# Kernel optimization log

Measured on AMD Instinct MI355X. Metric: run time of the kernel, lower is better.

## Reference

```python
import jax, jax.numpy as jnp
import numpy as np

P = 8  # patch_size hard-coded in the module


def conv1x1(x, W, b):
    # x: [B,C,H,W_], W: [O,C], b: [O]  (1x1 conv == per-pixel linear)
    return jnp.einsum('oc,bchw->bohw', W, x) + b[None, :, None, None]


def to_patch_tokens(t):
    # Replicates t.unfold(2,P,P).unfold(3,P,P).contiguous().view(B,-1,N)
    # t: [B,Cq,W,H] -> [B, Cq*P*P, N] with N = (W//P)*(H//P)
    B, Cq, Wd, Hd = t.shape
    Wp, Hp = Wd // P, Hd // P
    t = t.reshape(B, Cq, Wp, P, Hp, P).transpose(0, 1, 2, 4, 3, 5)  # [B,Cq,Wp,Hp,P,P]
    return t.reshape(B, Cq * P * P, Wp * Hp)


def setup_inputs() -> dict:
    key = jax.random.key(0)
    ks = jax.random.split(key, 10)
    B, C, Wd, Hd = 8, 64, 256, 256
    Cq = C // 8
    s_in = 1.0 / np.sqrt(C)
    s_out = 1.0 / np.sqrt(Cq)
    return {
        'x': jax.random.normal(ks[0], (B, C, Wd, Hd), jnp.float32),
        'Wq': jax.random.normal(ks[1], (Cq, C), jnp.float32) * s_in,
        'bq': jax.random.normal(ks[2], (Cq,), jnp.float32) * 0.01,
        'Wk': jax.random.normal(ks[3], (Cq, C), jnp.float32) * s_in,
        'bk': jax.random.normal(ks[4], (Cq,), jnp.float32) * 0.01,
        'Wv': jax.random.normal(ks[5], (Cq, C), jnp.float32) * s_in,
        'bv': jax.random.normal(ks[6], (Cq,), jnp.float32) * 0.01,
        'Wo': jax.random.normal(ks[7], (C, Cq), jnp.float32) * s_out,
        'bo': jax.random.normal(ks[8], (C,), jnp.float32) * 0.01,
        'gamma': jax.random.normal(ks[9], (1,), jnp.float32),
    }


def reference(x, Wq, bq, Wk, bk, Wv, bv, Wo, bo, gamma):
    B, C, Wd, Hd = x.shape
    Cq = C // 8
    q = to_patch_tokens(conv1x1(x, Wq, bq)).transpose(0, 2, 1)  # [B,N,M]
    k = to_patch_tokens(conv1x1(x, Wk, bk))                     # [B,M,N]
    v = to_patch_tokens(conv1x1(x, Wv, bv))                     # [B,M,N]
    N = k.shape[-1]  # d_k in source == number of patch tokens
    energy = jnp.einsum('bnm,bmk->bnk', q, k) / jnp.sqrt(jnp.float32(N))
    attn = jax.nn.softmax(energy, axis=-1)                      # [B,N,N]
    out = jnp.einsum('bmn,bjn->bmj', v, attn)                   # bmm(v, attn^T)
    out = out.transpose(0, 2, 1).reshape(B, Cq, Wd, Hd)
    out = conv1x1(out, Wo, bo)
    return gamma * out + x
```

## Files before the change

### kernel.cpp

```cpp
#include <hip/hip_runtime.h>
#include <stdint.h>

typedef unsigned short u16;
typedef unsigned int   u32;
typedef __attribute__((ext_vector_type(8))) short  short8;
typedef __attribute__((ext_vector_type(4))) float  floatx4;

__device__ __forceinline__ u16 f32_to_bf16(float f) {
  u32 u = __builtin_bit_cast(u32, f);
  u = (u + 0x7fffu + ((u >> 16) & 1u)) >> 16;
  return (u16)u;
}
__device__ __forceinline__ float bf16_to_f32(u16 h) {
  u32 u = ((u32)h) << 16;
  return __builtin_bit_cast(float, u);
}
__device__ __forceinline__ float bf16_lo(u32 u) {
  return __builtin_bit_cast(float, u << 16);
}
__device__ __forceinline__ float bf16_hi(u32 u) {
  return __builtin_bit_cast(float, u & 0xffff0000u);
}

__device__ __forceinline__ void load_lds16(const u16* g, u16* l) {
  auto gp = (const __attribute__((address_space(1))) u32*)(uintptr_t)g;
  auto lp = (__attribute__((address_space(3))) u32*)(u32)(uintptr_t)l;
  __builtin_amdgcn_global_load_lds(gp, lp, 16, 0, 0);
}

__global__ __launch_bounds__(512) void qkv_kernel(
    const float* __restrict__ x,
    const float* __restrict__ Wq, const float* __restrict__ bq,
    const float* __restrict__ Wk, const float* __restrict__ bk,
    const float* __restrict__ Wv, const float* __restrict__ bv,
    u16* __restrict__ qt, u16* __restrict__ kt, u16* __restrict__ vm)
{
  __shared__ __align__(16) u16 qs[128 * 64];
  __shared__ __align__(16) u16 ks_[128 * 64];
  __shared__ __align__(16) u16 vs[64 * 128];

  const int wq = blockIdx.x;
  const int g  = blockIdx.y;
  const int b  = blockIdx.z;
  const int t  = threadIdx.x;
  const int vt0 = t << 1;
  const int lw = vt0 >> 5, lh = vt0 & 31;
  const int w  = wq * 32 + lw;
  const int h  = g * 16 + (lh & 15) + ((lh >> 4) << 7);
  const int nl = ((lh >> 3) & 1) * 64 + (lw & 7) * 8 + (lh & 7);
  const int mc = ((lw >> 3) << 1) + (lh >> 4);

  float aq[2][8], ak[2][8], av[2][8];
#pragma unroll
  for (int j = 0; j < 2; j++)
#pragma unroll
    for (int i = 0; i < 8; i++) { aq[j][i] = 0.f; ak[j][i] = 0.f; av[j][i] = 0.f; }

  const float* xp = x + (size_t)b * 64 * 65536 + w * 256 + h;
#pragma unroll 4
  for (int c = 0; c < 64; c++) {
    float2 xv = *(const float2*)(xp + c * 65536);
#pragma unroll
    for (int cq = 0; cq < 8; cq++) {
      float wqc = Wq[cq * 64 + c], wkc = Wk[cq * 64 + c], wvc = Wv[cq * 64 + c];
      aq[0][cq] = fmaf(wqc, xv.x, aq[0][cq]);
      ak[0][cq] = fmaf(wkc, xv.x, ak[0][cq]);
      av[0][cq] = fmaf(wvc, xv.x, av[0][cq]);
      aq[1][cq] = fmaf(wqc, xv.y, aq[1][cq]);
      ak[1][cq] = fmaf(wkc, xv.y, ak[1][cq]);
      av[1][cq] = fmaf(wvc, xv.y, av[1][cq]);
    }
  }
#pragma unroll
  for (int j = 0; j < 2; j++)
#pragma unroll
    for (int cq = 0; cq < 8; cq++) {
      qs[(nl + j) * 64 + cq * 8 + mc]    = f32_to_bf16(aq[j][cq] + bq[cq]);
      ks_[(nl + j) * 64 + cq * 8 + mc]   = f32_to_bf16(ak[j][cq] + bk[cq]);
      vs[(cq * 8 + mc) * 128 + nl + j]   = f32_to_bf16(av[j][cq] + bv[cq]);
    }
  __syncthreads();

#pragma unroll
  for (int i = 0; i < 2; i++) {
    const int vt = t + i * 512;
    {
      const int nl2 = vt >> 3, cq2 = vt & 7;
      const size_t row = (size_t)b * 1024 + g * 128 + nl2;
      uint4 vq = *(const uint4*)(qs + nl2 * 64 + cq2 * 8);
      uint4 vk = *(const uint4*)(ks_ + nl2 * 64 + cq2 * 8);
      *(uint4*)(qt + row * 512 + cq2 * 64 + wq * 8) = vq;
      *(uint4*)(kt + row * 512 + cq2 * 64 + wq * 8) = vk;
    }
    {
      const int pr = vt >> 4, l16 = vt & 15;
      const int cq3 = pr >> 3, mc3 = pr & 7;
      const int mrow = cq3 * 64 + wq * 8 + mc3;
      uint4 vv = *(const uint4*)(vs + pr * 128 + l16 * 8);
      *(uint4*)(vm + ((size_t)b * 512 + mrow) * 1024 + g * 128 + l16 * 8) = vv;
    }
  }
}

template <int FMW>
__global__ __launch_bounds__(256) void gemm_nt(
    const u16* __restrict__ A, const u16* __restrict__ Bm, u16* __restrict__ Cm,
    int M, int N, int K, float scale)
{
  constexpr int BM = FMW * 32;
  __shared__ __align__(16) u16 As[BM * 64];
  __shared__ __align__(16) u16 Bs[128 * 64];

  const int bn = blockIdx.x, bm = blockIdx.y, bz = blockIdx.z;
  const int t = threadIdx.x;
  const int lane = t & 63, wid = t >> 6;
  const int wm = wid & 1, wn = wid >> 1;
  const int m0 = bm * BM, n0 = bn * 128;

  const u16* Ab = A + (size_t)bz * M * K + (size_t)m0 * K;
  const u16* Bb = Bm + (size_t)bz * N * K + (size_t)n0 * K;

  floatx4 acc[FMW][4];
#pragma unroll
  for (int i = 0; i < FMW; i++)
#pragma unroll
    for (int j = 0; j < 4; j++) acc[i][j] = (floatx4){0.f, 0.f, 0.f, 0.f};

  const int srow = wid * 8 + (lane >> 3);
  const int scol = (((lane & 7) ^ ((lane >> 3) & 7)) << 3);
  const int l15 = lane & 15, quad = lane >> 4;
  const int cxor = (l15 & 7) << 3;

  for (int k0 = 0; k0 < K; k0 += 64) {
#pragma unroll
    for (int i = 0; i < FMW; i++)
      load_lds16(Ab + (size_t)(i * 32 + srow) * K + k0 + scol, As + (i * 32 + wid * 8) * 64);
#pragma unroll
    for (int i = 0; i < 4; i++)
      load_lds16(Bb + (size_t)(i * 32 + srow) * K + k0 + scol, Bs + (i * 32 + wid * 8) * 64);
    __syncthreads();
#pragma unroll
    for (int ks = 0; ks < 2; ks++) {
      const int koff = (ks * 32 + quad * 8) ^ cxor;
      short8 a[FMW], b[4];
#pragma unroll
      for (int f = 0; f < FMW; f++)
        a[f] = *(const short8*)(As + (wm * FMW * 16 + f * 16 + l15) * 64 + koff);
#pragma unroll
      for (int f = 0; f < 4; f++)
        b[f] = *(const short8*)(Bs + (wn * 64 + f * 16 + l15) * 64 + koff);
#pragma unroll
      for (int fm = 0; fm < FMW; fm++)
#pragma unroll
        for (int fn = 0; fn < 4; fn++)
          acc[fm][fn] = __builtin_amdgcn_mfma_f32_16x16x32_bf16(a[fm], b[fn], acc[fm][fn], 0, 0, 0);
    }
    __syncthreads();
  }

  u16* Cb = Cm + (size_t)bz * M * N;
#pragma unroll
  for (int fm = 0; fm < FMW; fm++)
#pragma unroll
    for (int fn = 0; fn < 4; fn++)
#pragma unroll
      for (int r = 0; r < 4; r++) {
        int row = m0 + wm * FMW * 16 + fm * 16 + quad * 4 + r;
        int col = n0 + wn * 64 + fn * 16 + l15;
        Cb[(size_t)row * N + col] = f32_to_bf16(scale * acc[fm][fn][r]);
      }
}

__global__ __launch_bounds__(256) void softmax_kernel(u16* __restrict__ EP)
{
  const int lane = threadIdx.x & 63, wid = threadIdx.x >> 6;
  const int r = blockIdx.x * 4 + wid;
  u32* row = (u32*)(EP + (size_t)r * 1024);

  uint4 c0 = ((const uint4*)row)[lane];
  uint4 c1 = ((const uint4*)row)[64 + lane];
  u32 u[8] = {c0.x, c0.y, c0.z, c0.w, c1.x, c1.y, c1.z, c1.w};
  float e[16];
#pragma unroll
  for (int i = 0; i < 8; i++) { e[2 * i] = bf16_lo(u[i]); e[2 * i + 1] = bf16_hi(u[i]); }

  float mx = e[0];
#pragma unroll
  for (int i = 1; i < 16; i++) mx = fmaxf(mx, e[i]);
#pragma unroll
  for (int off = 32; off > 0; off >>= 1) mx = fmaxf(mx, __shfl_xor(mx, off));

  float s = 0.f;
#pragma unroll
  for (int i = 0; i < 16; i++) { e[i] = __expf(e[i] - mx); s += e[i]; }
#pragma unroll
  for (int off = 32; off > 0; off >>= 1) s += __shfl_xor(s, off);

  float inv = 1.0f / s;
#pragma unroll
  for (int i = 0; i < 8; i++)
    u[i] = (u32)f32_to_bf16(e[2 * i] * inv) | ((u32)f32_to_bf16(e[2 * i + 1] * inv) << 16);
  ((uint4*)row)[lane]      = (uint4){u[0], u[1], u[2], u[3]};
  ((uint4*)row)[64 + lane] = (uint4){u[4], u[5], u[6], u[7]};
}

__global__ __launch_bounds__(256) void out_kernel(
    const float* __restrict__ x, const u16* __restrict__ OT,
    const float* __restrict__ Wo, const float* __restrict__ bo,
    const float* __restrict__ gammap, float* __restrict__ out)
{
  const int tid = blockIdx.x * 256 + threadIdx.x;
  const int pix = tid << 2;
  const int b = pix >> 16, rem = pix & 65535;
  const float g = gammap[0];

  const u16* otb = OT + (size_t)b * 524288;
  const int m = rem & 511;
  const int nbase = rem >> 9;
  float oc[8][4];
#pragma unroll
  for (int cq = 0; cq < 8; cq++) {
    ushort4 hv = *(const ushort4*)(otb + (size_t)(cq * 128 + nbase) * 512 + m);
    oc[cq][0] = bf16_to_f32(hv.x); oc[cq][1] = bf16_to_f32(hv.y);
    oc[cq][2] = bf16_to_f32(hv.z); oc[cq][3] = bf16_to_f32(hv.w);
  }

  const float4* xb4 = (const float4*)(x + (size_t)b * 4194304 + rem);
  float4* ob4 = (float4*)(out + (size_t)b * 4194304 + rem);
#pragma unroll 4
  for (int o = 0; o < 64; o++) {
    float4 xv = xb4[o * 16384];
    float a0 = bo[o], a1 = a0, a2 = a0, a3 = a0;
#pragma unroll
    for (int cq = 0; cq < 8; cq++) {
      float wv = Wo[o * 8 + cq];
      a0 = fmaf(wv, oc[cq][0], a0);
      a1 = fmaf(wv, oc[cq][1], a1);
      a2 = fmaf(wv, oc[cq][2], a2);
      a3 = fmaf(wv, oc[cq][3], a3);
    }
    float4 r;
    r.x = fmaf(g, a0, xv.x); r.y = fmaf(g, a1, xv.y);
    r.z = fmaf(g, a2, xv.z); r.w = fmaf(g, a3, xv.w);
    ob4[o * 16384] = r;
  }
}

extern "C" void kernel_launch(void* const* d_in, const int* in_sizes, int n_in,
                              void* d_out, int out_size, void* d_ws, size_t ws_size,
                              hipStream_t stream) {
  const float* x  = (const float*)d_in[0];
  const float* Wq = (const float*)d_in[1];
  const float* bq = (const float*)d_in[2];
  const float* Wk = (const float*)d_in[3];
  const float* bk = (const float*)d_in[4];
  const float* Wv = (const float*)d_in[5];
  const float* bv = (const float*)d_in[6];
  const float* Wo = (const float*)d_in[7];
  const float* bo = (const float*)d_in[8];
  const float* gm = (const float*)d_in[9];
  float* out = (float*)d_out;

  u16* qt = (u16*)d_ws;
  u16* kt = qt + 4194304;
  u16* vm = kt + 4194304;
  u16* EP = vm + 4194304;
  u16* OT = qt;

  qkv_kernel<<<dim3(8, 8, 8), 512, 0, stream>>>(x, Wq, bq, Wk, bk, Wv, bv, qt, kt, vm);
  gemm_nt<4><<<dim3(8, 8, 8), 256, 0, stream>>>(qt, kt, EP, 1024, 1024, 512, 0.03125f);
  softmax_kernel<<<2048, 256, 0, stream>>>(EP);
  gemm_nt<2><<<dim3(4, 16, 8), 256, 0, stream>>>(EP, vm, OT, 1024, 512, 1024, 1.0f);
  out_kernel<<<512, 256, 0, stream>>>(x, OT, Wo, bo, gm, out);
}
```

Measured before the change: 340.8 us.

## Rewrite QKV projection with float4 loads, prefetch, and direct scattered stores

Restructures the QKV 1x1-conv kernel so each thread computes 4 contiguous pixels with float4 loads of x and a two-deep register prefetch across channels. It removes the LDS staging buffers and the block barrier, writing q/k as scattered 2-byte global stores and v as 8-byte stores directly into the patch-token layout. The grid becomes 512 blocks of 256 threads. Input reads get wider and the shared-memory pass goes away, but the output writes for q and k become uncoalesced narrow stores, and register use rises to 96 accumulators per thread.

```diff
diff --git a/kernel.cpp b/kernel.cpp
--- a/kernel.cpp
+++ b/kernel.cpp
@@ -28,77 +28,73 @@
   __builtin_amdgcn_global_load_lds(gp, lp, 16, 0, 0);
 }
 
-__global__ __launch_bounds__(512) void qkv_kernel(
+__global__ __launch_bounds__(256) void qkv_kernel(
     const float* __restrict__ x,
     const float* __restrict__ Wq, const float* __restrict__ bq,
     const float* __restrict__ Wk, const float* __restrict__ bk,
     const float* __restrict__ Wv, const float* __restrict__ bv,
     u16* __restrict__ qt, u16* __restrict__ kt, u16* __restrict__ vm)
 {
-  __shared__ __align__(16) u16 qs[128 * 64];
-  __shared__ __align__(16) u16 ks_[128 * 64];
-  __shared__ __align__(16) u16 vs[64 * 128];
-
-  const int wq = blockIdx.x;
-  const int g  = blockIdx.y;
-  const int b  = blockIdx.z;
-  const int t  = threadIdx.x;
-  const int vt0 = t << 1;
-  const int lw = vt0 >> 5, lh = vt0 & 31;
-  const int w  = wq * 32 + lw;
-  const int h  = g * 16 + (lh & 15) + ((lh >> 4) << 7);
-  const int nl = ((lh >> 3) & 1) * 64 + (lw & 7) * 8 + (lh & 7);
-  const int mc = ((lw >> 3) << 1) + (lh >> 4);
-
-  float aq[2][8], ak[2][8], av[2][8];
-#pragma unroll
-  for (int j = 0; j < 2; j++)
-#pragma unroll
-    for (int i = 0; i < 8; i++) { aq[j][i] = 0.f; ak[j][i] = 0.f; av[j][i] = 0.f; }
-
-  const float* xp = x + (size_t)b * 64 * 65536 + w * 256 + h;
-#pragma unroll 4
+  const int t = threadIdx.x;
+  const int wv = t >> 6, l = t & 63;
+  const int w = blockIdx.x * 4 + wv;
+  const int b = blockIdx.y;
+  const int h0 = l << 2;
+
+  const float4* xq = (const float4*)(x + (size_t)b * 4194304 + w * 256 + h0);
+
+  float aq[8][4], ak[8][4], av[8][4];
+#pragma unroll
+  for (int cq = 0; cq < 8; cq++)
+#pragma unroll
+    for (int p = 0; p < 4; p++) { aq[cq][p] = 0.f; ak[cq][p] = 0.f; av[cq][p] = 0.f; }
+
+  float4 x0 = xq[0];
+  float4 x1 = xq[16384];
+#pragma unroll 2
   for (int c = 0; c < 64; c++) {
-    float2 xv = *(const float2*)(xp + c * 65536);
+    float4 cur = x0;
+    x0 = x1;
+    int cn = c + 2 < 64 ? c + 2 : 63;
+    x1 = xq[(size_t)cn * 16384];
 #pragma unroll
     for (int cq = 0; cq < 8; cq++) {
       float wqc = Wq[cq * 64 + c], wkc = Wk[cq * 64 + c], wvc = Wv[cq * 64 + c];
-      aq[0][cq] = fmaf(wqc, xv.x, aq[0][cq]);
-      ak[0][cq] = fmaf(wkc, xv.x, ak[0][cq]);
-      av[0][cq] = fmaf(wvc, xv.x, av[0][cq]);
-      aq[1][cq] = fmaf(wqc, xv.y, aq[1][cq]);
-      ak[1][cq] = fmaf(wkc, xv.y, ak[1][cq]);
-      av[1][cq] = fmaf(wvc, xv.y, av[1][cq]);
-    }
-  }
-#pragma unroll
-  for (int j = 0; j < 2; j++)
-#pragma unroll
-    for (int cq = 0; cq < 8; cq++) {
-      qs[(nl + j) * 64 + cq * 8 + mc]    = f32_to_bf16(aq[j][cq] + bq[cq]);
-      ks_[(nl + j) * 64 + cq * 8 + mc]   = f32_to_bf16(ak[j][cq] + bk[cq]);
-      vs[(cq * 8 + mc) * 128 + nl + j]   = f32_to_bf16(av[j][cq] + bv[cq]);
-    }
-  __syncthreads();
-
-#pragma unroll
-  for (int i = 0; i < 2; i++) {
-    const int vt = t + i * 512;
-    {
-      const int nl2 = vt >> 3, cq2 = vt & 7;
-      const size_t row = (size_t)b * 1024 + g * 128 + nl2;
-      uint4 vq = *(const uint4*)(qs + nl2 * 64 + cq2 * 8);
-      uint4 vk = *(const uint4*)(ks_ + nl2 * 64 + cq2 * 8);
-      *(uint4*)(qt + row * 512 + cq2 * 64 + wq * 8) = vq;
-      *(uint4*)(kt + row * 512 + cq2 * 64 + wq * 8) = vk;
-    }
-    {
-      const int pr = vt >> 4, l16 = vt & 15;
-      const int cq3 = pr >> 3, mc3 = pr & 7;
-      const int mrow = cq3 * 64 + wq * 8 + mc3;
-      uint4 vv = *(const uint4*)(vs + pr * 128 + l16 * 8);
-      *(uint4*)(vm + ((size_t)b * 512 + mrow) * 1024 + g * 128 + l16 * 8) = vv;
-    }
+      aq[cq][0] = fmaf(wqc, cur.x, aq[cq][0]);
+      aq[cq][1] = fmaf(wqc, cur.y, aq[cq][1]);
+      aq[cq][2] = fmaf(wqc, cur.z, aq[cq][2]);
+      aq[cq][3] = fmaf(wqc, cur.w, aq[cq][3]);
+      ak[cq][0] = fmaf(wkc, cur.x, ak[cq][0]);
+      ak[cq][1] = fmaf(wkc, cur.y, ak[cq][1]);
+      ak[cq][2] = fmaf(wkc, cur.z, ak[cq][2]);
+      ak[cq][3] = fmaf(wkc, cur.w, ak[cq][3]);
+      av[cq][0] = fmaf(wvc, cur.x, av[cq][0]);
+      av[cq][1] = fmaf(wvc, cur.y, av[cq][1]);
+      av[cq][2] = fmaf(wvc, cur.z, av[cq][2]);
+      av[cq][3] = fmaf(wvc, cur.w, av[cq][3]);
+    }
+  }
+
+  const int hh = l >> 5;
+  const int Mb = ((w >> 3) << 1) + hh;
+  const int N0 = ((l >> 2) & 7) * 128 + ((l >> 1) & 1) * 64 + (w & 7) * 8 + ((l & 1) << 2);
+  const size_t qtbase = ((size_t)b * 1024 + N0) * 512 + Mb;
+
+#pragma unroll
+  for (int cq = 0; cq < 8; cq++) {
+    const float bqc = bq[cq], bkc = bk[cq], bvc = bv[cq];
+    const size_t o = qtbase + cq * 64;
+#pragma unroll
+    for (int j = 0; j < 4; j++) {
+      qt[o + (size_t)j * 512] = f32_to_bf16(aq[cq][j] + bqc);
+      kt[o + (size_t)j * 512] = f32_to_bf16(ak[cq][j] + bkc);
+    }
+    ushort4 pv;
+    pv.x = f32_to_bf16(av[cq][0] + bvc);
+    pv.y = f32_to_bf16(av[cq][1] + bvc);
+    pv.z = f32_to_bf16(av[cq][2] + bvc);
+    pv.w = f32_to_bf16(av[cq][3] + bvc);
+    *(ushort4*)(vm + ((size_t)b * 512 + cq * 64 + Mb) * 1024 + N0) = pv;
   }
 }
 
@@ -267,7 +263,7 @@
   u16* EP = vm + 4194304;
   u16* OT = qt;
 
-  qkv_kernel<<<dim3(8, 8, 8), 512, 0, stream>>>(x, Wq, bq, Wk, bk, Wv, bv, qt, kt, vm);
+  qkv_kernel<<<dim3(64, 8), 256, 0, stream>>>(x, Wq, bq, Wk, bk, Wv, bv, qt, kt, vm);
   gemm_nt<4><<<dim3(8, 8, 8), 256, 0, stream>>>(qt, kt, EP, 1024, 1024, 512, 0.03125f);
   softmax_kernel<<<2048, 256, 0, stream>>>(EP);
   gemm_nt<2><<<dim3(4, 16, 8), 256, 0, stream>>>(EP, vm, OT, 1024, 512, 1024, 1.0f);
```

After: 363.6 us. +6.7%, slower.
